# Performance work log

Hardware: AMD Instinct MI355X
Metric: run time of the kernel (lower is better)

Reference implementation:

```python
import jax, jax.numpy as jnp
import numpy as np

N, HID, NC, GD, HEADS = 8192, 768, 18, 256, 2
K = 5            # knn_k in the module
E_CLS = 324      # class co-occurrence edges (<= 18*18)
NEG_SLOPE = 0.2  # GATv2Conv default
EPS = 1e-5       # LayerNorm eps


def _ln(x, g, b):
    m = x.mean(-1, keepdims=True)
    v = ((x - m) ** 2).mean(-1, keepdims=True)
    return (x - m) / jnp.sqrt(v + EPS) * g + b


def _seg_softmax(scores, seg, n):
    # softmax over edges grouped by destination node (irregular segments)
    m = jax.ops.segment_max(scores, seg, num_segments=n)
    e = jnp.exp(scores - m[seg])
    s = jax.ops.segment_sum(e, seg, num_segments=n)
    return e / s[seg]


def _gatv2(x, src, dst, wl, bl, wr, br, att, bias, n):
    # PyG GATv2Conv (heads=2, concat=True), eval mode (dropout off)
    xl = (x @ wl.T + bl).reshape(n, HEADS, GD)   # lin_l -> source features
    xr = (x @ wr.T + br).reshape(n, HEADS, GD)   # lin_r -> target features
    h = jax.nn.leaky_relu(xl[src] + xr[dst], NEG_SLOPE)     # [E,H,D]
    scores = jnp.einsum('ehd,hd->eh', h, att)               # [E,H]
    alpha = _seg_softmax(scores, dst, n)
    out = jax.ops.segment_sum(xl[src] * alpha[..., None], dst, num_segments=n)
    return out.reshape(n, HEADS * GD) + bias


def _add_self_loops(src, dst, n):
    # GATv2Conv default add_self_loops=True
    loops = jnp.arange(n)
    return jnp.concatenate([src, loops]), jnp.concatenate([dst, loops])


def _knn_edges(x, k):
    # torch_cluster knn_graph(x, k, loop=True): self-distance 0 is always kept
    x2 = jnp.sum(x * x, -1)
    d = x2[:, None] + x2[None, :] - 2.0 * (x @ x.T)  # [N,N] sq. distances
    _, idx = jax.lax.top_k(-d, k)                    # k nearest incl. self
    src = idx.reshape(-1)                            # neighbors (sources)
    dst = jnp.repeat(jnp.arange(x.shape[0]), k)      # centers (targets)
    return src, dst


def _forward(class_edge_index, instance_features, class_emb,
             gc_wl, gc_bl, gc_wr, gc_br, gc_att, gc_bias,
             gi_wl, gi_bl, gi_wr, gi_br, gi_att, gi_bias,
             q_w, q_b, ctx_w, ctx_b, wv, bv, wo, bo, ln1_g, ln1_b,
             ln2_g, ln2_b, gw_w, gw_b, temperature):
    n = instance_features.shape[0]
    # class graph GATv2
    csrc, cdst = _add_self_loops(class_edge_index[0], class_edge_index[1], NC)
    class_feat = _gatv2(class_emb, csrc, cdst, gc_wl, gc_bl, gc_wr, gc_br,
                        gc_att, gc_bias, NC)                  # [NC, 512]
    # kNN graph + instance GATv2
    isrc, idst = _knn_edges(instance_features, K)
    isrc, idst = _add_self_loops(isrc, idst, n)
    gnn_inst = _gatv2(instance_features, isrc, idst, gi_wl, gi_bl, gi_wr,
                      gi_br, gi_att, gi_bias, n)              # [N, 512]
    ctx = class_feat.mean(0, keepdims=True) + gnn_inst        # [N, 512]
    # cross-attention fusion: q/k/v have seq_len 1, so softmax == 1 and the
    # MHA output reduces to out_proj(v_proj(context_proj(ctx))); query path
    # (q_w, q_b) cancels out of the forward value.
    ctx_p = ctx @ ctx_w.T + ctx_b                             # [N, 768]
    attn = (ctx_p @ wv.T + bv) @ wo.T + bo                    # [N, 768]
    fused = _ln(instance_features + attn, ln1_g, ln1_b)
    # pre_classifier: LayerNorm -> GELU (exact) -> Dropout(eval)
    pre = jax.nn.gelu(_ln(fused, ln2_g, ln2_b), approximate=False)
    # GroupWiseLinear
    logits = jnp.einsum('ch,nh->nc', gw_w[0], pre) + gw_b[0]
    return logits / temperature  # eval-mode temperature scaling


def setup_inputs() -> dict:
    key = jax.random.key(0)
    ks = jax.random.split(key, 32)
    rn = lambda i, shape, s: jax.random.normal(ks[i], shape, jnp.float32) * s
    inp = {
        'instance_features': jax.random.normal(ks[0], (N, HID), jnp.float32),
        'class_edge_index': jax.random.randint(ks[1], (2, E_CLS), 0, NC),
        'class_emb': rn(2, (NC, HID), 0.02),
        'gc_wl': rn(3, (HEADS * GD, HID), 0.02), 'gc_bl': jnp.zeros(HEADS * GD),
        'gc_wr': rn(4, (HEADS * GD, HID), 0.02), 'gc_br': jnp.zeros(HEADS * GD),
        'gc_att': rn(5, (HEADS, GD), 0.1), 'gc_bias': jnp.zeros(HEADS * GD),
        'gi_wl': rn(6, (HEADS * GD, HID), 0.02), 'gi_bl': jnp.zeros(HEADS * GD),
        'gi_wr': rn(7, (HEADS * GD, HID), 0.02), 'gi_br': jnp.zeros(HEADS * GD),
        'gi_att': rn(8, (HEADS, GD), 0.1), 'gi_bias': jnp.zeros(HEADS * GD),
        'q_w': rn(9, (HID, HID), 0.02), 'q_b': jnp.zeros(HID),
        'ctx_w': rn(10, (HID, HEADS * GD), 0.02), 'ctx_b': jnp.zeros(HID),
        'wv': rn(11, (HID, HID), 0.02), 'bv': jnp.zeros(HID),
        'wo': rn(12, (HID, HID), 0.02), 'bo': jnp.zeros(HID),
        'ln1_g': jnp.ones(HID), 'ln1_b': jnp.zeros(HID),
        'ln2_g': jnp.ones(HID), 'ln2_b': jnp.zeros(HID),
        'gw_w': rn(13, (1, NC, HID), 0.036), 'gw_b': jnp.zeros((1, NC)),
        'temperature': jnp.ones(1),
    }
    return inp


def reference(instance_features, class_edge_index, class_emb,
              gc_wl, gc_bl, gc_wr, gc_br, gc_att, gc_bias,
              gi_wl, gi_bl, gi_wr, gi_br, gi_att, gi_bias,
              q_w, q_b, ctx_w, ctx_b, wv, bv, wo, bo, ln1_g, ln1_b,
              ln2_g, ln2_b, gw_w, gw_b, temperature):
    return _forward(class_edge_index, instance_features, class_emb,
                    gc_wl, gc_bl, gc_wr, gc_br, gc_att, gc_bias,
                    gi_wl, gi_bl, gi_wr, gi_br, gi_att, gi_bias,
                    q_w, q_b, ctx_w, ctx_b, wv, bv, wo, bo, ln1_g, ln1_b,
                    ln2_g, ln2_b, gw_w, gw_b, temperature)
```

## Files before the change

### kernel.cpp

```cpp
#include <hip/hip_runtime.h>
#include <hip/hip_bf16.h>
#include <hip/hip_fp16.h>
#include <math.h>

#define NN 8192
#define HIDD 768
#define NCLS 18
#define OD 512
#define ETOT 342
#define NEG 0.2f
#define LN_EPS 1e-5f

typedef __attribute__((ext_vector_type(8))) short bf16x8;
typedef __attribute__((ext_vector_type(4))) float f32x4;

__device__ __forceinline__ void top5_insert(float s, int idx,
    float& d0, float& d1, float& d2, float& d3, float& d4,
    int& i0, int& i1, int& i2, int& i3, int& i4) {
  if (s >= d4) return;
  if (s < d3) {
    d4 = d3; i4 = i3;
    if (s < d2) {
      d3 = d2; i3 = i2;
      if (s < d1) {
        d2 = d1; i2 = i1;
        if (s < d0) { d1 = d0; i1 = i0; d0 = s; i0 = idx; }
        else        { d1 = s;  i1 = idx; }
      } else { d2 = s; i2 = idx; }
    } else { d3 = s; i3 = idx; }
  } else { d4 = s; i4 = idx; }
}

__device__ __forceinline__ void top8k_insert(unsigned key, unsigned (&kk)[8]) {
  if (key >= kk[7]) return;
  int rank = 0;
  #pragma unroll
  for (int k = 0; k < 7; ++k) rank += (key >= kk[k]) ? 1 : 0;
  #pragma unroll
  for (int k = 7; k >= 1; --k) if (k > rank) kk[k] = kk[k-1];
  #pragma unroll
  for (int k = 0; k < 8; ++k) if (k == rank) kk[k] = key;
}

__device__ __forceinline__ void stage16(const void* g, void* l) {
  __builtin_amdgcn_global_load_lds(
      (const __attribute__((address_space(1))) unsigned int*)g,
      (__attribute__((address_space(3))) unsigned int*)l, 16, 0, 0);
}

__device__ __forceinline__ ushort f2b(float v) {
  __hip_bfloat16 b = __float2bfloat16(v);
  return *(ushort*)&b;
}

__global__ __launch_bounds__(256) void prep1_kernel(
    const float* __restrict__ X, ushort* __restrict__ Xh, float* __restrict__ x2,
    const float* __restrict__ gi_wl, const float* __restrict__ gi_wr,
    ushort* __restrict__ wlrh,
    const float* __restrict__ cemb, const float* __restrict__ gc_wl,
    const float* __restrict__ gc_bl, const float* __restrict__ gc_wr,
    const float* __restrict__ gc_br, float* __restrict__ xlc, float* __restrict__ xrc,
    const float* __restrict__ wv, const float* __restrict__ ctx_b,
    const float* __restrict__ bv, float* __restrict__ t1b,
    const float* __restrict__ gi_bl, const float* __restrict__ gi_br,
    float* __restrict__ bb) {
  const int bx = blockIdx.x, tid = threadIdx.x;
  if (bx < 2048) {
    const int row = bx * 4 + (tid >> 6);
    const int lane = tid & 63;
    const float4* src = (const float4*)(X + (size_t)row * HIDD);
    ushort4* dst = (ushort4*)(Xh + (size_t)row * HIDD);
    float s = 0.f;
    #pragma unroll
    for (int q = 0; q < 3; ++q) {
      float4 v = src[lane + q * 64];
      s += v.x * v.x + v.y * v.y + v.z * v.z + v.w * v.w;
      dst[lane + q * 64] = make_ushort4(f2b(v.x), f2b(v.y), f2b(v.z), f2b(v.w));
    }
    #pragma unroll
    for (int off = 32; off; off >>= 1) s += __shfl_down(s, off);
    if (lane == 0) x2[row] = s;
  } else if (bx < 2816) {
    int rel = bx - 2048;
    const float* src = gi_wl; ushort* dst = wlrh;
    if (rel >= 384) { rel -= 384; src = gi_wr; dst = wlrh + (size_t)OD * HIDD; }
    const int i = rel * 256 + tid;
    float4 v = ((const float4*)src)[i];
    ((ushort4*)dst)[i] = make_ushort4(f2b(v.x), f2b(v.y), f2b(v.z), f2b(v.w));
  } else if (bx < 2888) {
    int t = (bx - 2816) * 256 + tid;
    const float* W; const float* b; float* Y;
    if (t < NCLS * OD) { W = gc_wl; b = gc_bl; Y = xlc; }
    else { t -= NCLS * OD; W = gc_wr; b = gc_br; Y = xrc; }
    const int row = t / OD, o = t - row * OD;
    const float4* xr4 = (const float4*)(cemb + (size_t)row * HIDD);
    const float4* wr4 = (const float4*)(W + (size_t)o * HIDD);
    float acc = 0.f;
    for (int k = 0; k < HIDD / 4; ++k) {
      const float4 a = xr4[k], w4 = wr4[k];
      acc += a.x * w4.x + a.y * w4.y + a.z * w4.z + a.w * w4.w;
    }
    Y[t] = acc + b[o];
  } else if (bx < 2891) {
    const int t = (bx - 2888) * 256 + tid;
    if (t < HIDD) {
      const float4* cb4 = (const float4*)ctx_b;
      const float4* wv4 = (const float4*)(wv + (size_t)t * HIDD);
      float acc = 0.f;
      for (int k = 0; k < HIDD / 4; ++k) {
        const float4 a = cb4[k], w4 = wv4[k];
        acc += a.x * w4.x + a.y * w4.y + a.z * w4.z + a.w * w4.w;
      }
      t1b[t] = acc + bv[t];
    }
  } else {
    const int t = (bx - 2891) * 256 + tid;
    if (t < OD) bb[t] = gi_bl[t];
    else if (t < 2 * OD) bb[t] = gi_br[t - OD];
  }
}

__global__ __launch_bounds__(256) void gemm_nn_f32(const float* __restrict__ A,
    const float* __restrict__ B, float* __restrict__ Cf, ushort* __restrict__ Ch,
    int M, int N, int K) {
  __shared__ float As[64][33];
  __shared__ float Bs[32][65];
  const int tid = threadIdx.x, tx = tid & 15, ty = tid >> 4;
  const int r0 = blockIdx.x * 64, c0 = blockIdx.y * 64;
  float acc[4][4] = {};
  for (int kt = 0; kt < K; kt += 32) {
    __syncthreads();
    #pragma unroll
    for (int l = 0; l < 8; ++l) {
      const int idx = l * 256 + tid;
      const int m = idx >> 5, k = idx & 31;
      As[m][k] = A[(size_t)(r0 + m) * K + kt + k];
      const int k2 = idx >> 6, n = idx & 63;
      Bs[k2][n] = B[(size_t)(kt + k2) * N + c0 + n];
    }
    __syncthreads();
    #pragma unroll
    for (int k = 0; k < 32; ++k) {
      float a[4], b[4];
      #pragma unroll
      for (int i = 0; i < 4; ++i) a[i] = As[ty * 4 + i][k];
      #pragma unroll
      for (int j = 0; j < 4; ++j) b[j] = Bs[k][tx * 4 + j];
      #pragma unroll
      for (int i = 0; i < 4; ++i)
        #pragma unroll
        for (int j = 0; j < 4; ++j) acc[i][j] += a[i] * b[j];
    }
  }
  #pragma unroll
  for (int i = 0; i < 4; ++i) {
    const int r = r0 + ty * 4 + i;
    #pragma unroll
    for (int j = 0; j < 4; ++j) {
      const int c = c0 + tx * 4 + j;
      if (Ch) Ch[(size_t)r * N + c] = f2b(acc[i][j]);
      else    Cf[(size_t)r * N + c] = acc[i][j];
    }
  }
}

__global__ __launch_bounds__(256) void prep2_kernel(
    const float* __restrict__ wo, const float* __restrict__ t1b,
    const float* __restrict__ bo, float* __restrict__ bp,
    const int* __restrict__ cei, const float* __restrict__ xlc,
    const float* __restrict__ xrc, const float* __restrict__ gc_att,
    const float* __restrict__ gc_bias, float* __restrict__ cmean) {
  __shared__ float sc[ETOT * 2];
  __shared__ int es[ETOT], ed[ETOT];
  __shared__ float mx[NCLS][2], sm[NCLS][2];
  const int bx = blockIdx.x, tid = threadIdx.x;
  if (bx < 3) {
    const int t = bx * 256 + tid;
    if (t < HIDD) {
      const float4* tb4 = (const float4*)t1b;
      const float4* wo4 = (const float4*)(wo + (size_t)t * HIDD);
      float acc = 0.f;
      for (int k = 0; k < HIDD / 4; ++k) {
        const float4 a = tb4[k], w4 = wo4[k];
        acc += a.x * w4.x + a.y * w4.y + a.z * w4.z + a.w * w4.w;
      }
      bp[t] = acc + bo[t];
    }
  } else {
    for (int e = tid; e < ETOT; e += 256) {
      if (e < 324) { es[e] = cei[e]; ed[e] = cei[324 + e]; }
      else         { es[e] = e - 324; ed[e] = e - 324; }
    }
    __syncthreads();
    const int lane = tid & 63, w = tid >> 6;
    for (int t = w; t < ETOT * 2; t += 4) {
      const int e = t >> 1, h = t & 1;
      const float* xlr = xlc + (size_t)es[e] * OD + h * 256;
      const float* xrr = xrc + (size_t)ed[e] * OD + h * 256;
      const float* ar  = gc_att + h * 256;
      float s = 0.f;
      for (int d = lane; d < 256; d += 64) {
        float v = xlr[d] + xrr[d];
        v = v > 0.f ? v : NEG * v;
        s += v * ar[d];
      }
      #pragma unroll
      for (int off = 32; off; off >>= 1) s += __shfl_down(s, off);
      if (lane == 0) sc[t] = s;
    }
    __syncthreads();
    if (tid < NCLS * 2) {
      const int d = tid >> 1, h = tid & 1;
      float m = -3e38f;
      for (int e = 0; e < ETOT; ++e) if (ed[e] == d) m = fmaxf(m, sc[e * 2 + h]);
      float ssum = 0.f;
      for (int e = 0; e < ETOT; ++e) if (ed[e] == d) ssum += expf(sc[e * 2 + h] - m);
      mx[d][h] = m; sm[d][h] = 1.f / ssum;
    }
    __syncthreads();
    for (int t = tid; t < ETOT * 2; t += 256) {
      const int e = t >> 1, h = t & 1;
      sc[t] = expf(sc[t] - mx[ed[e]][h]) * sm[ed[e]][h];
    }
    __syncthreads();
    for (int c = tid; c < OD; c += 256) {
      const int h = c >> 8;
      float acc = 0.f;
      for (int e = 0; e < ETOT; ++e) acc += sc[e * 2 + h] * xlc[(size_t)es[e] * OD + c];
      cmean[c] = acc * (1.f / 18.f) + gc_bias[c];
    }
  }
}

__global__ __launch_bounds__(256, 4) void dist_sym_mfma(
    const ushort* __restrict__ Xh, const float* __restrict__ x2,
    unsigned* __restrict__ pck) {
  __shared__ __align__(16) char lds[32768];
  __shared__ float x2i[128], x2j[128];
  char* const sA = lds;
  char* const sB = lds + 16384;
  __half* const Dh = (__half*)lds;
  unsigned* const ck = (unsigned*)lds;

  const int t = blockIdx.x;
  int by = (int)((sqrtf(8.0f * (float)t + 1.0f) - 1.0f) * 0.5f);
  while ((by + 1) * (by + 2) / 2 <= t) ++by;
  while (by * (by + 1) / 2 > t) --by;
  const int bx = t - by * (by + 1) / 2;

  const int tid = threadIdx.x;
  const int lane = tid & 63, wid = tid >> 6;
  const int fr = lane & 15, fq = lane >> 4;
  const int i0 = bx * 128, j0 = by * 128;
  const int wr = (wid >> 1) * 64, wc = (wid & 1) * 64;
  const bool diag = (bx == by);

  if (tid < 128) x2i[tid] = x2[i0 + tid];
  else x2j[tid - 128] = x2[j0 + tid - 128];

  f32x4 acc[4][4] = {};
  for (int kt = 0; kt < HIDD; kt += 64) {
    __syncthreads();
    #pragma unroll
    for (int q = 0; q < 4; ++q) {
      const int chunkid = q * 256 + tid;
      const int row = chunkid >> 3, cc = chunkid & 7;
      const bf16x8 va = *(const bf16x8*)(Xh + (size_t)(i0 + row) * HIDD + kt + cc * 8);
      const bf16x8 vb = *(const bf16x8*)(Xh + (size_t)(j0 + row) * HIDD + kt + cc * 8);
      const int wi = row * 128 + ((cc ^ (row & 7)) << 4);
      *(bf16x8*)(sA + wi) = va;
      *(bf16x8*)(sB + wi) = vb;
    }
    __syncthreads();
    #pragma unroll
    for (int kk = 0; kk < 2; ++kk) {
      bf16x8 bh[4];
      #pragma unroll
      for (int n = 0; n < 4; ++n) {
        const int br = wc + n * 16 + fr;
        bh[n] = *(const bf16x8*)(sB + br * 128 + (((kk * 4 + fq) ^ (br & 7)) << 4));
      }
      #pragma unroll
      for (int m = 0; m < 4; ++m) {
        const int ar = wr + m * 16 + fr;
        const bf16x8 a = *(const bf16x8*)(sA + ar * 128 + (((kk * 4 + fq) ^ (ar & 7)) << 4));
        #pragma unroll
        for (int n = 0; n < 4; ++n)
          acc[m][n] = __builtin_amdgcn_mfma_f32_16x16x32_bf16(a, bh[n], acc[m][n], 0, 0, 0);
      }
    }
  }
  __syncthreads();
  #pragma unroll
  for (int n = 0; n < 4; ++n) {
    const int col = wc + n * 16 + fr;
    #pragma unroll
    for (int m = 0; m < 4; ++m) {
      #pragma unroll
      for (int j = 0; j < 4; ++j) {
        const int row = wr + m * 16 + fq * 4 + j;
        Dh[row * 128 + ((col + row) & 127)] = __float2half(-2.0f * acc[m][n][j]);
      }
    }
  }
  __syncthreads();

  unsigned ki[8], kj[8];
  #pragma unroll
  for (int k = 0; k < 8; ++k) { ki[k] = 0xFFFFFFFFu; kj[k] = 0xFFFFFFFFu; }
  const int r = tid & 127, h = tid >> 7;
  for (int c = 0; c < 64; ++c) {
    const int col = h * 64 + c;
    const float s = x2j[col] - 768.0f + __half2float(Dh[r * 128 + ((col + r) & 127)]);
    const ushort u = __half_as_ushort(__float2half(s));
    const ushort k16 = (u & 0x8000) ? (ushort)(~u) : (ushort)(u | 0x8000);
    top8k_insert(((unsigned)k16 << 16) | (unsigned)(j0 + col), ki);
  }
  if (!diag) {
    for (int c = 0; c < 64; ++c) {
      const int cr = h * 64 + c;
      const float s = x2i[cr] - 768.0f + __half2float(Dh[cr * 128 + ((r + cr) & 127)]);
      const ushort u = __half_as_ushort(__float2half(s));
      const ushort k16 = (u & 0x8000) ? (ushort)(~u) : (ushort)(u | 0x8000);
      top8k_insert(((unsigned)k16 << 16) | (unsigned)(i0 + cr), kj);
    }
  }
  __syncthreads();
  #pragma unroll
  for (int k = 0; k < 8; ++k) ck[tid * 8 + k] = ki[k];
  __syncthreads();
  if (tid < 128) {
    unsigned mk[8];
    #pragma unroll
    for (int k = 0; k < 8; ++k) mk[k] = ck[tid * 8 + k];
    #pragma unroll
    for (int k = 0; k < 8; ++k) top8k_insert(ck[(tid + 128) * 8 + k], mk);
    const size_t base = ((size_t)(i0 + tid) * 64 + by) * 8;
    #pragma unroll
    for (int k = 0; k < 8; ++k) pck[base + k] = mk[k];
  }
  if (!diag) {
    __syncthreads();
    #pragma unroll
    for (int k = 0; k < 8; ++k) ck[tid * 8 + k] = kj[k];
    __syncthreads();
    if (tid < 128) {
      unsigned mk[8];
      #pragma unroll
      for (int k = 0; k < 8; ++k) mk[k] = ck[tid * 8 + k];
      #pragma unroll
      for (int k = 0; k < 8; ++k) top8k_insert(ck[(tid + 128) * 8 + k], mk);
      const size_t base = ((size_t)(j0 + tid) * 64 + bx) * 8;
      #pragma unroll
      for (int k = 0; k < 8; ++k) pck[base + k] = mk[k];
    }
  }
}

__global__ __launch_bounds__(256) void merge_refine_kernel(
    const float* __restrict__ X, const float* __restrict__ x2,
    const unsigned* __restrict__ pck, int* __restrict__ knn) {
  const int row = blockIdx.x * 4 + (threadIdx.x >> 6);
  const int lane = threadIdx.x & 63;
  unsigned mk[8];
  #pragma unroll
  for (int k = 0; k < 8; ++k) mk[k] = pck[(size_t)row * 512 + lane * 8 + k];
  #pragma unroll
  for (int st = 1; st < 64; st <<= 1) {
    unsigned ok[8];
    #pragma unroll
    for (int k = 0; k < 8; ++k) ok[k] = __shfl_xor(mk[k], st);
    #pragma unroll
    for (int k = 0; k < 8; ++k) top8k_insert(ok[k], mk);
  }
  int c[8];
  #pragma unroll
  for (int k = 0; k < 8; ++k) c[k] = (int)(mk[k] & 0xFFFFu);
  const float4* xi = (const float4*)(X + (size_t)row * HIDD);
  float acc[8] = {};
  #pragma unroll
  for (int q = 0; q < 3; ++q) {
    const float4 a = xi[lane + q * 64];
    #pragma unroll
    for (int k = 0; k < 8; ++k) {
      const float4 b = ((const float4*)(X + (size_t)c[k] * HIDD))[lane + q * 64];
      acc[k] += a.x * b.x + a.y * b.y + a.z * b.z + a.w * b.w;
    }
  }
  #pragma unroll
  for (int k = 0; k < 8; ++k) {
    #pragma unroll
    for (int off = 32; off; off >>= 1) acc[k] += __shfl_down(acc[k], off);
  }
  if (lane == 0) {
    float d0 = 3e38f, d1 = 3e38f, d2 = 3e38f, d3 = 3e38f, d4 = 3e38f;
    int i0 = 0, i1 = 0, i2 = 0, i3 = 0, i4 = 0;
    #pragma unroll
    for (int k = 0; k < 8; ++k) {
      const float s = x2[c[k]] - 2.0f * acc[k];
      top5_insert(s, c[k], d0, d1, d2, d3, d4, i0, i1, i2, i3, i4);
    }
    knn[row * 5 + 0] = i0; knn[row * 5 + 1] = i1; knn[row * 5 + 2] = i2;
    knn[row * 5 + 3] = i3; knn[row * 5 + 4] = i4;
  }
}

__global__ __launch_bounds__(256) void gemm_nt_mfma(const ushort* __restrict__ A,
    const ushort* __restrict__ B, const float* __restrict__ bias,
    float* __restrict__ C, int Nc, int K) {
  __shared__ char lds[32768];
  char* const pA = lds;
  char* const pB = lds + 16384;
  const int tid = threadIdx.x;
  const int lane = tid & 63, wid = tid >> 6;
  const int fr = lane & 15, fq = lane >> 4;
  const int r0 = blockIdx.x * 128;
  const int c0 = blockIdx.y * 128;
  const int wr = (wid >> 1) * 64, wc = (wid & 1) * 64;
  f32x4 acc[4][4] = {};
  for (int kt = 0; kt < K; kt += 64) {
    __syncthreads();
    #pragma unroll
    for (int q = 0; q < 4; ++q) {
      const int chunk = wid * 256 + q * 64 + lane;
      const int row = chunk >> 3;
      const int lc = (chunk & 7) ^ (row & 7);
      const int ld = wid * 4096 + q * 1024;
      stage16((const char*)A + ((size_t)(r0 + row) * K + kt) * 2 + (size_t)lc * 16, pA + ld);
      stage16((const char*)B + ((size_t)(c0 + row) * K + kt) * 2 + (size_t)lc * 16, pB + ld);
    }
    __syncthreads();
    #pragma unroll
    for (int kk = 0; kk < 2; ++kk) {
      bf16x8 ah[4], bh[4];
      #pragma unroll
      for (int m = 0; m < 4; ++m) {
        const int ar = wr + m * 16 + fr;
        ah[m] = *(const bf16x8*)(pA + ar * 128 + (((kk * 4 + fq) ^ (ar & 7)) << 4));
      }
      #pragma unroll
      for (int n = 0; n < 4; ++n) {
        const int br = wc + n * 16 + fr;
        bh[n] = *(const bf16x8*)(pB + br * 128 + (((kk * 4 + fq) ^ (br & 7)) << 4));
      }
      #pragma unroll
      for (int m = 0; m < 4; ++m)
        #pragma unroll
        for (int n = 0; n < 4; ++n)
          acc[m][n] = __builtin_amdgcn_mfma_f32_16x16x32_bf16(ah[m], bh[n], acc[m][n], 0, 0, 0);
    }
  }
  #pragma unroll
  for (int n = 0; n < 4; ++n) {
    const int cc = c0 + wc + n * 16 + fr;
    const float bs = bias[cc];
    #pragma unroll
    for (int m = 0; m < 4; ++m) {
      #pragma unroll
      for (int j = 0; j < 4; ++j) {
        const int rr = r0 + wr + m * 16 + fq * 4 + j;
        C[(size_t)rr * Nc + cc] = acc[m][n][j] + bs;
      }
    }
  }
}

__global__ __launch_bounds__(256) void inst_gat_kernel(const float* __restrict__ xlr,
    const int* __restrict__ knn, const float* __restrict__ att,
    const float* __restrict__ bias, const float* __restrict__ cmean,
    ushort* __restrict__ ctxh) {
  __shared__ float rows[7][512];
  __shared__ float sc[12];
  __shared__ float alpha[12];
  __shared__ int nbr[6];
  const int i = blockIdx.x;
  const int tid = threadIdx.x;
  if (tid < 5) nbr[tid] = knn[i * 5 + tid];
  else if (tid == 5) nbr[5] = i;
  __syncthreads();
  for (int t = tid; t < 7 * 128; t += 256) {
    const int rr = t >> 7, e4 = t & 127;
    const float* src = (rr < 6) ? (xlr + (size_t)nbr[rr] * 1024)
                                : (xlr + (size_t)i * 1024 + 512);
    ((float4*)rows[rr])[e4] = ((const float4*)src)[e4];
  }
  __syncthreads();
  const int lane = tid & 63, w = tid >> 6;
  for (int t = w; t < 12; t += 4) {
    const int e = t >> 1, h = t & 1;
    const float* ar = att + h * 256;
    float s = 0.f;
    #pragma unroll
    for (int q = 0; q < 4; ++q) {
      const int d = lane + q * 64;
      float v = rows[e][h * 256 + d] + rows[6][h * 256 + d];
      v = v > 0.f ? v : NEG * v;
      s += v * ar[d];
    }
    #pragma unroll
    for (int off = 32; off; off >>= 1) s += __shfl_down(s, off);
    if (lane == 0) sc[t] = s;
  }
  __syncthreads();
  if (tid < 2) {
    const int h = tid;
    float m = -3e38f;
    #pragma unroll
    for (int e = 0; e < 6; ++e) m = fmaxf(m, sc[e * 2 + h]);
    float ssum = 0.f;
    #pragma unroll
    for (int e = 0; e < 6; ++e) { float ex = expf(sc[e * 2 + h] - m); alpha[e * 2 + h] = ex; ssum += ex; }
    const float inv = 1.f / ssum;
    #pragma unroll
    for (int e = 0; e < 6; ++e) alpha[e * 2 + h] *= inv;
  }
  __syncthreads();
  for (int c = tid; c < OD; c += 256) {
    const int h = c >> 8;
    float acc = 0.f;
    #pragma unroll
    for (int e = 0; e < 6; ++e) acc += alpha[e * 2 + h] * rows[e][c];
    ctxh[(size_t)i * OD + c] = f2b(acc + bias[c] + cmean[c]);
  }
}

__global__ __launch_bounds__(256) void epilogue_kernel(const float* __restrict__ inst,
    const float* __restrict__ attn, const float* __restrict__ g1, const float* __restrict__ b1,
    const float* __restrict__ g2, const float* __restrict__ b2, const float* __restrict__ gw,
    const float* __restrict__ gb, const float* __restrict__ temp, float* __restrict__ out) {
  __shared__ float buf[HIDD];
  __shared__ float red[4];
  const int i = blockIdx.x;
  const int tid = threadIdx.x;
  const int lane = tid & 63, w = tid >> 6;
  size_t base = (size_t)i * HIDD;
  float v0 = inst[base + tid]       + attn[base + tid];
  float v1 = inst[base + tid + 256] + attn[base + tid + 256];
  float v2 = inst[base + tid + 512] + attn[base + tid + 512];

  float s = v0 + v1 + v2;
  #pragma unroll
  for (int off = 32; off; off >>= 1) s += __shfl_down(s, off);
  if (lane == 0) red[w] = s;
  __syncthreads();
  float mean = (red[0] + red[1] + red[2] + red[3]) * (1.f / HIDD);
  __syncthreads();
  float e0 = v0 - mean, e1 = v1 - mean, e2 = v2 - mean;
  s = e0 * e0 + e1 * e1 + e2 * e2;
  #pragma unroll
  for (int off = 32; off; off >>= 1) s += __shfl_down(s, off);
  if (lane == 0) red[w] = s;
  __syncthreads();
  float rstd = rsqrtf((red[0] + red[1] + red[2] + red[3]) * (1.f / HIDD) + LN_EPS);
  __syncthreads();
  float y0 = e0 * rstd * g1[tid]       + b1[tid];
  float y1 = e1 * rstd * g1[tid + 256] + b1[tid + 256];
  float y2 = e2 * rstd * g1[tid + 512] + b1[tid + 512];

  s = y0 + y1 + y2;
  #pragma unroll
  for (int off = 32; off; off >>= 1) s += __shfl_down(s, off);
  if (lane == 0) red[w] = s;
  __syncthreads();
  float mean2 = (red[0] + red[1] + red[2] + red[3]) * (1.f / HIDD);
  __syncthreads();
  float f0 = y0 - mean2, f1 = y1 - mean2, f2 = y2 - mean2;
  s = f0 * f0 + f1 * f1 + f2 * f2;
  #pragma unroll
  for (int off = 32; off; off >>= 1) s += __shfl_down(s, off);
  if (lane == 0) red[w] = s;
  __syncthreads();
  float rstd2 = rsqrtf((red[0] + red[1] + red[2] + red[3]) * (1.f / HIDD) + LN_EPS);
  float z0 = f0 * rstd2 * g2[tid]       + b2[tid];
  float z1 = f1 * rstd2 * g2[tid + 256] + b2[tid + 256];
  float z2 = f2 * rstd2 * g2[tid + 512] + b2[tid + 512];
  buf[tid]       = 0.5f * z0 * (1.f + erff(z0 * 0.70710678118654752f));
  buf[tid + 256] = 0.5f * z1 * (1.f + erff(z1 * 0.70710678118654752f));
  buf[tid + 512] = 0.5f * z2 * (1.f + erff(z2 * 0.70710678118654752f));
  __syncthreads();

  float invT = 1.f / temp[0];
  for (int c = w; c < NCLS; c += 4) {
    const float* wr = gw + (size_t)c * HIDD;
    float acc = 0.f;
    for (int d = lane; d < HIDD; d += 64) acc += buf[d] * wr[d];
    #pragma unroll
    for (int off = 32; off; off >>= 1) acc += __shfl_down(acc, off);
    if (lane == 0) out[(size_t)i * NCLS + c] = (acc + gb[c]) * invT;
  }
}

extern "C" void kernel_launch(void* const* d_in, const int* in_sizes, int n_in,
                              void* d_out, int out_size, void* d_ws, size_t ws_size,
                              hipStream_t stream) {
  (void)in_sizes; (void)n_in; (void)out_size; (void)ws_size;
  const float* X       = (const float*)d_in[0];
  const int*   cei     = (const int*)  d_in[1];
  const float* cemb    = (const float*)d_in[2];
  const float* gc_wl   = (const float*)d_in[3];
  const float* gc_bl   = (const float*)d_in[4];
  const float* gc_wr   = (const float*)d_in[5];
  const float* gc_br   = (const float*)d_in[6];
  const float* gc_att  = (const float*)d_in[7];
  const float* gc_bias = (const float*)d_in[8];
  const float* gi_wl   = (const float*)d_in[9];
  const float* gi_bl   = (const float*)d_in[10];
  const float* gi_wr   = (const float*)d_in[11];
  const float* gi_br   = (const float*)d_in[12];
  const float* gi_att  = (const float*)d_in[13];
  const float* gi_bias = (const float*)d_in[14];
  const float* ctx_w   = (const float*)d_in[17];
  const float* ctx_b   = (const float*)d_in[18];
  const float* wv      = (const float*)d_in[19];
  const float* bv      = (const float*)d_in[20];
  const float* wo      = (const float*)d_in[21];
  const float* bo      = (const float*)d_in[22];
  const float* ln1_g   = (const float*)d_in[23];
  const float* ln1_b   = (const float*)d_in[24];
  const float* ln2_g   = (const float*)d_in[25];
  const float* ln2_b   = (const float*)d_in[26];
  const float* gw_w    = (const float*)d_in[27];
  const float* gw_b    = (const float*)d_in[28];
  const float* temp    = (const float*)d_in[29];
  float* out = (float*)d_out;

  float* ws  = (float*)d_ws;
  float* R1  = ws;
  float* R2  = R1 + (size_t)NN * OD;
  float* R3  = R2 + (size_t)NN * OD;
  float* R4  = R3 + (size_t)NN * OD;

  float* x2    = R4;
  ushort* w3h  = (ushort*)(x2 + NN);
  float* t1b   = (float*)(w3h + (size_t)HIDD * OD);
  float* bp    = t1b + HIDD;
  float* bb    = bp + HIDD;
  int*   knn   = (int*)(bb + 2 * OD);
  float* xlc   = (float*)(knn + NN * 5);
  float* xrc   = xlc + NCLS * OD;
  float* cmean = xrc + NCLS * OD;

  unsigned* pck = (unsigned*)R1;
  float* xlr   = R1;
  float* attnb = R1;
  float* T1    = R2;
  ushort* Xh   = (ushort*)R3;
  ushort* wlrh = (ushort*)(R3 + (size_t)NN * HIDD / 2);
  ushort* ctxh = (ushort*)R3;

  prep1_kernel<<<2895, 256, 0, stream>>>(X, Xh, x2, gi_wl, gi_wr, wlrh,
      cemb, gc_wl, gc_bl, gc_wr, gc_br, xlc, xrc,
      wv, ctx_b, bv, t1b, gi_bl, gi_br, bb);
  gemm_nn_f32<<<dim3(HIDD / 64, OD / 64), 256, 0, stream>>>(wv, ctx_w, T1, nullptr, HIDD, OD, HIDD);
  gemm_nn_f32<<<dim3(HIDD / 64, OD / 64), 256, 0, stream>>>(wo, T1, nullptr, w3h, HIDD, OD, HIDD);
  prep2_kernel<<<4, 256, 0, stream>>>(wo, t1b, bo, bp, cei, xlc, xrc, gc_att, gc_bias, cmean);
  dist_sym_mfma<<<2080, 256, 0, stream>>>(Xh, x2, pck);
  merge_refine_kernel<<<NN / 4, 256, 0, stream>>>(X, x2, pck, knn);
  gemm_nt_mfma<<<dim3(NN / 128, (2 * OD) / 128), 256, 0, stream>>>(Xh, wlrh, bb, xlr, 2 * OD, HIDD);
  inst_gat_kernel<<<NN, 256, 0, stream>>>(xlr, knn, gi_att, gi_bias, cmean, ctxh);
  gemm_nt_mfma<<<dim3(NN / 128, HIDD / 128), 256, 0, stream>>>(ctxh, w3h, bp, attnb, HIDD, OD);
  epilogue_kernel<<<NN, 256, 0, stream>>>(X, attnb, ln1_g, ln1_b, ln2_g, ln2_b, gw_w, gw_b, temp, out);
}
```

Baseline: 762.8 us.

## Fuse kNN merge/refine into instance GAT kernel and store xl/xr as bf16

Merges the kNN candidate merge/refine step and the instance GATv2 attention into one per-node kernel, so the knn index array no longer goes through global memory and one launch is removed. The xl/xr projection GEMM now writes bf16 instead of fp32, halving its output traffic and the gather reads in the GAT step. The GEMM moves ahead of the distance kernel and the workspace aliasing is reshuffled to fit. Risks are lower precision in the attention inputs and a per-node block that now does serial merge work in one wave while the other three waves sit idle.

```diff
diff --git a/kernel.cpp b/kernel.cpp
--- a/kernel.cpp
+++ b/kernel.cpp
@@ -51,6 +51,10 @@
 __device__ __forceinline__ ushort f2b(float v) {
   __hip_bfloat16 b = __float2bfloat16(v);
   return *(ushort*)&b;
+}
+__device__ __forceinline__ float b2f(ushort u) {
+  unsigned uv = ((unsigned)u) << 16;
+  return *(float*)&uv;
 }
 
 __global__ __launch_bounds__(256) void prep1_kernel(
@@ -357,57 +361,119 @@
   }
 }
 
-__global__ __launch_bounds__(256) void merge_refine_kernel(
+__global__ __launch_bounds__(256) void mr_gat_kernel(
     const float* __restrict__ X, const float* __restrict__ x2,
-    const unsigned* __restrict__ pck, int* __restrict__ knn) {
-  const int row = blockIdx.x * 4 + (threadIdx.x >> 6);
-  const int lane = threadIdx.x & 63;
-  unsigned mk[8];
-  #pragma unroll
-  for (int k = 0; k < 8; ++k) mk[k] = pck[(size_t)row * 512 + lane * 8 + k];
-  #pragma unroll
-  for (int st = 1; st < 64; st <<= 1) {
-    unsigned ok[8];
-    #pragma unroll
-    for (int k = 0; k < 8; ++k) ok[k] = __shfl_xor(mk[k], st);
-    #pragma unroll
-    for (int k = 0; k < 8; ++k) top8k_insert(ok[k], mk);
-  }
-  int c[8];
-  #pragma unroll
-  for (int k = 0; k < 8; ++k) c[k] = (int)(mk[k] & 0xFFFFu);
-  const float4* xi = (const float4*)(X + (size_t)row * HIDD);
-  float acc[8] = {};
-  #pragma unroll
-  for (int q = 0; q < 3; ++q) {
-    const float4 a = xi[lane + q * 64];
-    #pragma unroll
-    for (int k = 0; k < 8; ++k) {
-      const float4 b = ((const float4*)(X + (size_t)c[k] * HIDD))[lane + q * 64];
-      acc[k] += a.x * b.x + a.y * b.y + a.z * b.z + a.w * b.w;
-    }
-  }
-  #pragma unroll
-  for (int k = 0; k < 8; ++k) {
-    #pragma unroll
-    for (int off = 32; off; off >>= 1) acc[k] += __shfl_down(acc[k], off);
-  }
-  if (lane == 0) {
+    const unsigned* __restrict__ pck, const ushort* __restrict__ xlrh,
+    const float* __restrict__ att, const float* __restrict__ bias,
+    const float* __restrict__ cmean, ushort* __restrict__ ctxh) {
+  __shared__ float rows[7][512];
+  __shared__ float rsc[8];
+  __shared__ int rcand[8];
+  __shared__ int nbr[6];
+  __shared__ float sc[12];
+  __shared__ float alpha[12];
+  const int i = blockIdx.x;
+  const int tid = threadIdx.x;
+  const int lane = tid & 63, w = tid >> 6;
+
+  if (w == 0) {
+    unsigned mk[8];
+    #pragma unroll
+    for (int k = 0; k < 8; ++k) mk[k] = pck[(size_t)i * 512 + lane * 8 + k];
+    #pragma unroll
+    for (int st = 1; st < 64; st <<= 1) {
+      unsigned ok[8];
+      #pragma unroll
+      for (int k = 0; k < 8; ++k) ok[k] = __shfl_xor(mk[k], st);
+      #pragma unroll
+      for (int k = 0; k < 8; ++k) top8k_insert(ok[k], mk);
+    }
+    if (lane < 8) rcand[lane] = (int)(mk[lane] & 0xFFFFu);
+  } else {
+    const int tt = tid - 64;
+    if (tt < 128) {
+      const int rr = 5 + (tt >> 6), e4 = tt & 63;
+      const bf16x8 v = *(const bf16x8*)(xlrh + (size_t)i * 1024 + (rr == 6 ? 512 : 0) + e4 * 8);
+      #pragma unroll
+      for (int j = 0; j < 8; ++j) rows[rr][e4 * 8 + j] = b2f((ushort)v[j]);
+    }
+  }
+  __syncthreads();
+  {
+    const int cnd = w * 2 + (lane >> 5);
+    const int sl = lane & 31;
+    const int cidx = rcand[cnd];
+    const float4* xi = (const float4*)(X + (size_t)i * HIDD);
+    const float4* xc = (const float4*)(X + (size_t)cidx * HIDD);
+    float acc = 0.f;
+    #pragma unroll
+    for (int q = 0; q < 6; ++q) {
+      const float4 a = xi[sl + q * 32];
+      const float4 b = xc[sl + q * 32];
+      acc += a.x * b.x + a.y * b.y + a.z * b.z + a.w * b.w;
+    }
+    #pragma unroll
+    for (int off = 16; off; off >>= 1) acc += __shfl_down(acc, off, 32);
+    if (sl == 0) rsc[cnd] = x2[cidx] - 2.0f * acc;
+  }
+  __syncthreads();
+  if (tid == 0) {
     float d0 = 3e38f, d1 = 3e38f, d2 = 3e38f, d3 = 3e38f, d4 = 3e38f;
     int i0 = 0, i1 = 0, i2 = 0, i3 = 0, i4 = 0;
     #pragma unroll
-    for (int k = 0; k < 8; ++k) {
-      const float s = x2[c[k]] - 2.0f * acc[k];
-      top5_insert(s, c[k], d0, d1, d2, d3, d4, i0, i1, i2, i3, i4);
-    }
-    knn[row * 5 + 0] = i0; knn[row * 5 + 1] = i1; knn[row * 5 + 2] = i2;
-    knn[row * 5 + 3] = i3; knn[row * 5 + 4] = i4;
+    for (int k = 0; k < 8; ++k)
+      top5_insert(rsc[k], rcand[k], d0, d1, d2, d3, d4, i0, i1, i2, i3, i4);
+    nbr[0] = i0; nbr[1] = i1; nbr[2] = i2; nbr[3] = i3; nbr[4] = i4; nbr[5] = i;
+  }
+  __syncthreads();
+  for (int t2 = tid; t2 < 5 * 64; t2 += 256) {
+    const int rr = t2 >> 6, e4 = t2 & 63;
+    const bf16x8 v = *(const bf16x8*)(xlrh + (size_t)nbr[rr] * 1024 + e4 * 8);
+    #pragma unroll
+    for (int j = 0; j < 8; ++j) rows[rr][e4 * 8 + j] = b2f((ushort)v[j]);
+  }
+  __syncthreads();
+  for (int t = w; t < 12; t += 4) {
+    const int e = t >> 1, h = t & 1;
+    const float* ar = att + h * 256;
+    float s = 0.f;
+    #pragma unroll
+    for (int q = 0; q < 4; ++q) {
+      const int d = lane + q * 64;
+      float v = rows[e][h * 256 + d] + rows[6][h * 256 + d];
+      v = v > 0.f ? v : NEG * v;
+      s += v * ar[d];
+    }
+    #pragma unroll
+    for (int off = 32; off; off >>= 1) s += __shfl_down(s, off);
+    if (lane == 0) sc[t] = s;
+  }
+  __syncthreads();
+  if (tid < 2) {
+    const int h = tid;
+    float m = -3e38f;
+    #pragma unroll
+    for (int e = 0; e < 6; ++e) m = fmaxf(m, sc[e * 2 + h]);
+    float ssum = 0.f;
+    #pragma unroll
+    for (int e = 0; e < 6; ++e) { float ex = expf(sc[e * 2 + h] - m); alpha[e * 2 + h] = ex; ssum += ex; }
+    const float inv = 1.f / ssum;
+    #pragma unroll
+    for (int e = 0; e < 6; ++e) alpha[e * 2 + h] *= inv;
+  }
+  __syncthreads();
+  for (int c = tid; c < OD; c += 256) {
+    const int h = c >> 8;
+    float acc = 0.f;
+    #pragma unroll
+    for (int e = 0; e < 6; ++e) acc += alpha[e * 2 + h] * rows[e][c];
+    ctxh[(size_t)i * OD + c] = f2b(acc + bias[c] + cmean[c]);
   }
 }
 
 __global__ __launch_bounds__(256) void gemm_nt_mfma(const ushort* __restrict__ A,
     const ushort* __restrict__ B, const float* __restrict__ bias,
-    float* __restrict__ C, int Nc, int K) {
+    float* __restrict__ C, ushort* __restrict__ Cb, int Nc, int K) {
   __shared__ char lds[32768];
   char* const pA = lds;
   char* const pB = lds + 16384;
@@ -459,68 +525,11 @@
       #pragma unroll
       for (int j = 0; j < 4; ++j) {
         const int rr = r0 + wr + m * 16 + fq * 4 + j;
-        C[(size_t)rr * Nc + cc] = acc[m][n][j] + bs;
-      }
-    }
-  }
-}
-
-__global__ __launch_bounds__(256) void inst_gat_kernel(const float* __restrict__ xlr,
-    const int* __restrict__ knn, const float* __restrict__ att,
-    const float* __restrict__ bias, const float* __restrict__ cmean,
-    ushort* __restrict__ ctxh) {
-  __shared__ float rows[7][512];
-  __shared__ float sc[12];
-  __shared__ float alpha[12];
-  __shared__ int nbr[6];
-  const int i = blockIdx.x;
-  const int tid = threadIdx.x;
-  if (tid < 5) nbr[tid] = knn[i * 5 + tid];
-  else if (tid == 5) nbr[5] = i;
-  __syncthreads();
-  for (int t = tid; t < 7 * 128; t += 256) {
-    const int rr = t >> 7, e4 = t & 127;
-    const float* src = (rr < 6) ? (xlr + (size_t)nbr[rr] * 1024)
-                                : (xlr + (size_t)i * 1024 + 512);
-    ((float4*)rows[rr])[e4] = ((const float4*)src)[e4];
-  }
-  __syncthreads();
-  const int lane = tid & 63, w = tid >> 6;
-  for (int t = w; t < 12; t += 4) {
-    const int e = t >> 1, h = t & 1;
-    const float* ar = att + h * 256;
-    float s = 0.f;
-    #pragma unroll
-    for (int q = 0; q < 4; ++q) {
-      const int d = lane + q * 64;
-      float v = rows[e][h * 256 + d] + rows[6][h * 256 + d];
-      v = v > 0.f ? v : NEG * v;
-      s += v * ar[d];
-    }
-    #pragma unroll
-    for (int off = 32; off; off >>= 1) s += __shfl_down(s, off);
-    if (lane == 0) sc[t] = s;
-  }
-  __syncthreads();
-  if (tid < 2) {
-    const int h = tid;
-    float m = -3e38f;
-    #pragma unroll
-    for (int e = 0; e < 6; ++e) m = fmaxf(m, sc[e * 2 + h]);
-    float ssum = 0.f;
-    #pragma unroll
-    for (int e = 0; e < 6; ++e) { float ex = expf(sc[e * 2 + h] - m); alpha[e * 2 + h] = ex; ssum += ex; }
-    const float inv = 1.f / ssum;
-    #pragma unroll
-    for (int e = 0; e < 6; ++e) alpha[e * 2 + h] *= inv;
-  }
-  __syncthreads();
-  for (int c = tid; c < OD; c += 256) {
-    const int h = c >> 8;
-    float acc = 0.f;
-    #pragma unroll
-    for (int e = 0; e < 6; ++e) acc += alpha[e * 2 + h] * rows[e][c];
-    ctxh[(size_t)i * OD + c] = f2b(acc + bias[c] + cmean[c]);
+        const float val = acc[m][n][j] + bs;
+        if (Cb) Cb[(size_t)rr * Nc + cc] = f2b(val);
+        else    C[(size_t)rr * Nc + cc] = val;
+      }
+    }
   }
 }
 
@@ -635,18 +644,17 @@
   float* t1b   = (float*)(w3h + (size_t)HIDD * OD);
   float* bp    = t1b + HIDD;
   float* bb    = bp + HIDD;
-  int*   knn   = (int*)(bb + 2 * OD);
-  float* xlc   = (float*)(knn + NN * 5);
+  float* xlc   = bb + 2 * OD;
   float* xrc   = xlc + NCLS * OD;
   float* cmean = xrc + NCLS * OD;
 
-  unsigned* pck = (unsigned*)R1;
-  float* xlr   = R1;
-  float* attnb = R1;
-  float* T1    = R2;
-  ushort* Xh   = (ushort*)R3;
-  ushort* wlrh = (ushort*)(R3 + (size_t)NN * HIDD / 2);
-  ushort* ctxh = (ushort*)R3;
+  float* T1     = R1;
+  ushort* xlrh  = (ushort*)R1;
+  float* attnb  = R1;
+  unsigned* pck = (unsigned*)R2;
+  ushort* Xh    = (ushort*)R3;
+  ushort* wlrh  = (ushort*)(R3 + (size_t)NN * HIDD / 2);
+  ushort* ctxh  = (ushort*)R3;
 
   prep1_kernel<<<2895, 256, 0, stream>>>(X, Xh, x2, gi_wl, gi_wr, wlrh,
       cemb, gc_wl, gc_bl, gc_wr, gc_br, xlc, xrc,
@@ -654,10 +662,9 @@
   gemm_nn_f32<<<dim3(HIDD / 64, OD / 64), 256, 0, stream>>>(wv, ctx_w, T1, nullptr, HIDD, OD, HIDD);
   gemm_nn_f32<<<dim3(HIDD / 64, OD / 64), 256, 0, stream>>>(wo, T1, nullptr, w3h, HIDD, OD, HIDD);
   prep2_kernel<<<4, 256, 0, stream>>>(wo, t1b, bo, bp, cei, xlc, xrc, gc_att, gc_bias, cmean);
+  gemm_nt_mfma<<<dim3(NN / 128, (2 * OD) / 128), 256, 0, stream>>>(Xh, wlrh, bb, nullptr, xlrh, 2 * OD, HIDD);
   dist_sym_mfma<<<2080, 256, 0, stream>>>(Xh, x2, pck);
-  merge_refine_kernel<<<NN / 4, 256, 0, stream>>>(X, x2, pck, knn);
-  gemm_nt_mfma<<<dim3(NN / 128, (2 * OD) / 128), 256, 0, stream>>>(Xh, wlrh, bb, xlr, 2 * OD, HIDD);
-  inst_gat_kernel<<<NN, 256, 0, stream>>>(xlr, knn, gi_att, gi_bias, cmean, ctxh);
-  gemm_nt_mfma<<<dim3(NN / 128, HIDD / 128), 256, 0, stream>>>(ctxh, w3h, bp, attnb, HIDD, OD);
+  mr_gat_kernel<<<NN, 256, 0, stream>>>(X, x2, pck, xlrh, gi_att, gi_bias, cmean, ctxh);
+  gemm_nt_mfma<<<dim3(NN / 128, HIDD / 128), 256, 0, stream>>>(ctxh, w3h, bp, attnb, nullptr, HIDD, OD);
   epilogue_kernel<<<NN, 256, 0, stream>>>(X, attnb, ln1_g, ln1_b, ln2_g, ln2_b, gw_w, gw_b, temp, out);
 }
```

Result: slower. 786.8 us (+3.1%).
